# Kernel tuning notes

Measured on AMD Instinct MI355X. Metric: run time of the kernel, lower is better.

Reference implementation:

```python
import jax, jax.numpy as jnp
import numpy as np

N = 40000
E = 640000
D_IN = 128
HID = 128


def _sage_conv(x_src, x_dst, edge_index, W_l, b_l, W_r):
    """PyG SAGEConv with mean aggregation.
    out = lin_l(mean_{j in N(i)} x_src[j]) + lin_r(x_dst[i])
    (lin_l carries the bias; lin_r has bias=False in PyG.)
    """
    src, dst = edge_index[0], edge_index[1]
    n = x_dst.shape[0]
    # gather neighbor (source) features, scatter-sum to targets
    msg_sum = jax.ops.segment_sum(x_src[src], dst, num_segments=n)  # [N, d]
    deg = jax.ops.segment_sum(jnp.ones((src.shape[0],), x_src.dtype), dst,
                              num_segments=n)  # [N]
    agg = msg_sum / jnp.maximum(deg, 1.0)[:, None]  # mean over in-neighbors
    return agg @ W_l + b_l + x_dst @ W_r


def setup_inputs() -> dict:
    key = jax.random.key(0)
    ks = jax.random.split(key, 8)
    s_in = 1.0 / np.sqrt(D_IN)
    s_h = 1.0 / np.sqrt(HID)
    return {
        "x": jax.random.normal(ks[0], (N, D_IN), jnp.float32),
        "edge_index": jax.random.randint(ks[1], (2, E), 0, N, jnp.int64)
                      if jax.config.jax_enable_x64 else
                      jax.random.randint(ks[1], (2, E), 0, N, jnp.int32),
        "W1_l": jax.random.normal(ks[2], (D_IN, HID), jnp.float32) * s_in,
        "b1": jax.random.normal(ks[3], (HID,), jnp.float32) * s_in,
        "W1_r": jax.random.normal(ks[4], (D_IN, HID), jnp.float32) * s_in,
        "W2_l": jax.random.normal(ks[5], (HID, HID), jnp.float32) * s_h,
        "b2": jax.random.normal(ks[6], (HID,), jnp.float32) * s_h,
        "W2_r": jax.random.normal(ks[7], (HID, HID), jnp.float32) * s_h,
    }


def reference(x, edge_index, W1_l, b1, W1_r, W2_l, b2, W2_r):
    h = _sage_conv(x, x, edge_index, W1_l, b1, W1_r)
    h = jax.nn.relu(h)
    out = _sage_conv(h, h, edge_index, W2_l, b2, W2_r)
    return out
```

## Files before the change

### kernel.cpp

```cpp
#include <hip/hip_runtime.h>
#include <hip/hip_bf16.h>

#define NN 40000
#define NE 640000
#define DD 128
#define SLOT 128

typedef unsigned short u16;
typedef unsigned int u32;
typedef __attribute__((ext_vector_type(8))) short short8v;
typedef __attribute__((ext_vector_type(4))) float f32x4;

__device__ __forceinline__ u16 f2b(float f) {
  __hip_bfloat16 h = __float2bfloat16(f);
  return *reinterpret_cast<u16*>(&h);
}

#define TOB_N (NN * DD / 4)
#define WCVT_N 65536
__global__ void setup_kernel(const float* __restrict__ x,
                             const float* __restrict__ W1l, const float* __restrict__ W1r,
                             const float* __restrict__ W2l, const float* __restrict__ W2r,
                             u16* __restrict__ xb, u16* __restrict__ wt1,
                             u16* __restrict__ wt2, int* __restrict__ cnt) {
  int i = blockIdx.x * 256 + threadIdx.x;
  if (i < TOB_N) {
    float4 v = *(const float4*)(x + (size_t)i * 4);
    ushort4 o;
    o.x = f2b(v.x); o.y = f2b(v.y); o.z = f2b(v.z); o.w = f2b(v.w);
    *(ushort4*)(xb + (size_t)i * 4) = o;
  } else if (i < TOB_N + WCVT_N) {
    int j = i - TOB_N;
    int layer = j >> 15;
    int jj = j & 32767;
    int n = jj >> 8, k = jj & 255;
    const float* W = layer ? ((k < 128) ? W2l : W2r) : ((k < 128) ? W1l : W1r);
    u16* Wt = layer ? wt2 : wt1;
    Wt[jj] = f2b(W[(size_t)(k & 127) * 128 + n]);
  } else if (i < TOB_N + WCVT_N + NN) {
    cnt[i - TOB_N - WCVT_N] = 0;
  }
}

__global__ void fill2_kernel(const int* __restrict__ src, const int* __restrict__ dst,
                             int* __restrict__ cnt, int* __restrict__ csr) {
  int e = blockIdx.x * 256 + threadIdx.x;
  if (e < NE) {
    int d = dst[e];
    int p = atomicAdd(&cnt[d], 1);
    if (p < SLOT) csr[(size_t)d * SLOT + p] = src[e];
  }
}

template <int OUT_BF16, int RELU>
__global__ __launch_bounds__(1024) void fused_kernel(
    const u16* __restrict__ feat, const int* __restrict__ cnt,
    const int* __restrict__ csr, const u16* __restrict__ Wt,
    const float* __restrict__ bias, void* __restrict__ outp) {
  __shared__ u16 As[2][16][128];
  const int t = threadIdx.x;
  const int wv = t >> 6;
  const int lane = t & 63;
  const int li = lane & 15;
  const int eo = lane >> 4;
  const int node = blockIdx.x * 16 + wv;
  const int swz = (wv & 7) << 4;

  const int deg = cnt[node];
  const int n = (deg < SLOT) ? deg : SLOT;
  const float inv = 1.0f / (float)(deg > 1 ? deg : 1);

  if (eo == 1) {
    const uint4 s = *(const uint4*)(feat + (size_t)node * DD + li * 8);
    *(uint4*)((char*)&As[1][wv][0] + ((li * 16) ^ swz)) = s;
  }

  float acc[8] = {0.f, 0.f, 0.f, 0.f, 0.f, 0.f, 0.f, 0.f};
  const int* crow = csr + (size_t)node * SLOT;
  for (int e = eo; e < n; e += 4) {
    const int srcn = crow[e];
    const uint4 v = *(const uint4*)(feat + (size_t)srcn * DD + li * 8);
    acc[0] += __uint_as_float(v.x << 16);
    acc[1] += __uint_as_float(v.x & 0xffff0000u);
    acc[2] += __uint_as_float(v.y << 16);
    acc[3] += __uint_as_float(v.y & 0xffff0000u);
    acc[4] += __uint_as_float(v.z << 16);
    acc[5] += __uint_as_float(v.z & 0xffff0000u);
    acc[6] += __uint_as_float(v.w << 16);
    acc[7] += __uint_as_float(v.w & 0xffff0000u);
  }
#pragma unroll
  for (int j = 0; j < 8; ++j) acc[j] += __shfl_xor(acc[j], 16, 64);
#pragma unroll
  for (int j = 0; j < 8; ++j) acc[j] += __shfl_xor(acc[j], 32, 64);
  if (eo == 0) {
    u16 r8[8];
#pragma unroll
    for (int j = 0; j < 8; ++j) r8[j] = f2b(acc[j] * inv);
    uint4 o;
    o.x = (u32)r8[0] | ((u32)r8[1] << 16);
    o.y = (u32)r8[2] | ((u32)r8[3] << 16);
    o.z = (u32)r8[4] | ((u32)r8[5] << 16);
    o.w = (u32)r8[6] | ((u32)r8[7] << 16);
    *(uint4*)((char*)&As[0][wv][0] + ((li * 16) ^ swz)) = o;
  }
  __syncthreads();

  if (wv < 8) {
    const int r = li;
    const int g = eo;
    f32x4 acc2 = (f32x4){0.f, 0.f, 0.f, 0.f};
#pragma unroll
    for (int ks = 0; ks < 8; ++ks) {
      const int sel = ks >> 2;
      const int c0 = (ks & 3) * 32 + g * 8;
      const short8v afr =
          *(const short8v*)((const char*)&As[sel][r][0] + ((c0 * 2) ^ ((r & 7) << 4)));
      const short8v bfr =
          *(const short8v*)(Wt + (size_t)(wv * 16 + r) * 256 + ks * 32 + g * 8);
      acc2 = __builtin_amdgcn_mfma_f32_16x16x32_bf16(afr, bfr, acc2, 0, 0, 0);
    }
    const int col = wv * 16 + r;
    const float bv = bias[col];
#pragma unroll
    for (int reg = 0; reg < 4; ++reg) {
      const int row = blockIdx.x * 16 + g * 4 + reg;
      float o = acc2[reg] + bv;
      if (RELU) o = fmaxf(o, 0.f);
      if (OUT_BF16)
        ((u16*)outp)[(size_t)row * DD + col] = f2b(o);
      else
        ((float*)outp)[(size_t)row * DD + col] = o;
    }
  }
}

extern "C" void kernel_launch(void* const* d_in, const int* in_sizes, int n_in,
                              void* d_out, int out_size, void* d_ws, size_t ws_size,
                              hipStream_t stream) {
  const float* x = (const float*)d_in[0];
  const int* ei = (const int*)d_in[1];
  const int* srcv = ei;
  const int* dstv = ei + NE;
  const float* W1l = (const float*)d_in[2];
  const float* b1 = (const float*)d_in[3];
  const float* W1r = (const float*)d_in[4];
  const float* W2l = (const float*)d_in[5];
  const float* b2 = (const float*)d_in[6];
  const float* W2r = (const float*)d_in[7];
  float* out = (float*)d_out;

  char* ws = (char*)d_ws;
  int* cnt = (int*)(ws + 0);
  int* csr = (int*)(ws + 160256);
  u16* xb = (u16*)(ws + 20640256);
  u16* hb = (u16*)(ws + 30880256);
  u16* wt1 = (u16*)(ws + 41120256);
  u16* wt2 = (u16*)(ws + 41185792);

  const int nbS = (TOB_N + WCVT_N + NN + 255) / 256;
  const int nbE = NE / 256;

  setup_kernel<<<nbS, 256, 0, stream>>>(x, W1l, W1r, W2l, W2r, xb, wt1, wt2, cnt);
  fill2_kernel<<<nbE, 256, 0, stream>>>(srcv, dstv, cnt, csr);
  fused_kernel<1, 1><<<NN / 16, 1024, 0, stream>>>(xb, cnt, csr, wt1, b1, (void*)hb);
  fused_kernel<0, 0><<<NN / 16, 1024, 0, stream>>>(hb, cnt, csr, wt2, b2, (void*)out);
}
```

Measured before the change: 137.6 us.

## Process four nodes per wave in fused SAGE kernel with 256-thread blocks

Each wave now aggregates four destination nodes at once, keeping four sets of accumulators and issuing four independent gathers per iteration. Missing neighbours point at a zeroed padding row, which replaces per-edge branching. The block shrinks to 256 threads, and every wave now computes two MFMA column tiles instead of half the waves sitting idle. CSR writes become nontemporal stores. The intent is more memory-level parallelism and better MFMA utilisation, at the cost of higher register pressure and wasted loads when the four nodes have very different degrees.

```diff
diff --git a/kernel.cpp b/kernel.cpp
--- a/kernel.cpp
+++ b/kernel.cpp
@@ -22,7 +22,8 @@
                              const float* __restrict__ W1l, const float* __restrict__ W1r,
                              const float* __restrict__ W2l, const float* __restrict__ W2r,
                              u16* __restrict__ xb, u16* __restrict__ wt1,
-                             u16* __restrict__ wt2, int* __restrict__ cnt) {
+                             u16* __restrict__ wt2, int* __restrict__ cnt,
+                             u16* __restrict__ hb) {
   int i = blockIdx.x * 256 + threadIdx.x;
   if (i < TOB_N) {
     float4 v = *(const float4*)(x + (size_t)i * 4);
@@ -39,6 +40,11 @@
     Wt[jj] = f2b(W[(size_t)(k & 127) * 128 + n]);
   } else if (i < TOB_N + WCVT_N + NN) {
     cnt[i - TOB_N - WCVT_N] = 0;
+  } else if (i < TOB_N + WCVT_N + NN + 128) {
+    int j = i - TOB_N - WCVT_N - NN;
+    u32* p = (j < 64) ? ((u32*)(xb + (size_t)NN * DD) + j)
+                      : ((u32*)(hb + (size_t)NN * DD) + (j - 64));
+    *p = 0u;
   }
 }
 
@@ -48,84 +54,118 @@
   if (e < NE) {
     int d = dst[e];
     int p = atomicAdd(&cnt[d], 1);
-    if (p < SLOT) csr[(size_t)d * SLOT + p] = src[e];
+    if (p < SLOT) __builtin_nontemporal_store(src[e], &csr[(size_t)d * SLOT + p]);
   }
 }
 
 template <int OUT_BF16, int RELU>
-__global__ __launch_bounds__(1024) void fused_kernel(
+__global__ __launch_bounds__(256) void fused_kernel(
     const u16* __restrict__ feat, const int* __restrict__ cnt,
     const int* __restrict__ csr, const u16* __restrict__ Wt,
     const float* __restrict__ bias, void* __restrict__ outp) {
   __shared__ u16 As[2][16][128];
   const int t = threadIdx.x;
-  const int wv = t >> 6;
+  const int w = t >> 6;
   const int lane = t & 63;
   const int li = lane & 15;
   const int eo = lane >> 4;
-  const int node = blockIdx.x * 16 + wv;
-  const int swz = (wv & 7) << 4;
-
-  const int deg = cnt[node];
-  const int n = (deg < SLOT) ? deg : SLOT;
-  const float inv = 1.0f / (float)(deg > 1 ? deg : 1);
-
-  if (eo == 1) {
-    const uint4 s = *(const uint4*)(feat + (size_t)node * DD + li * 8);
-    *(uint4*)((char*)&As[1][wv][0] + ((li * 16) ^ swz)) = s;
-  }
-
-  float acc[8] = {0.f, 0.f, 0.f, 0.f, 0.f, 0.f, 0.f, 0.f};
-  const int* crow = csr + (size_t)node * SLOT;
-  for (int e = eo; e < n; e += 4) {
-    const int srcn = crow[e];
-    const uint4 v = *(const uint4*)(feat + (size_t)srcn * DD + li * 8);
-    acc[0] += __uint_as_float(v.x << 16);
-    acc[1] += __uint_as_float(v.x & 0xffff0000u);
-    acc[2] += __uint_as_float(v.y << 16);
-    acc[3] += __uint_as_float(v.y & 0xffff0000u);
-    acc[4] += __uint_as_float(v.z << 16);
-    acc[5] += __uint_as_float(v.z & 0xffff0000u);
-    acc[6] += __uint_as_float(v.w << 16);
-    acc[7] += __uint_as_float(v.w & 0xffff0000u);
-  }
-#pragma unroll
-  for (int j = 0; j < 8; ++j) acc[j] += __shfl_xor(acc[j], 16, 64);
-#pragma unroll
-  for (int j = 0; j < 8; ++j) acc[j] += __shfl_xor(acc[j], 32, 64);
+  const int tile = blockIdx.x * 16;
+  const int node0 = tile + w * 4;
+
+  {
+    const int j = w * 4 + eo;
+    const uint4 s = *(const uint4*)(feat + (size_t)(tile + j) * DD + li * 8);
+    *(uint4*)((char*)&As[1][j][0] + ((li * 16) ^ ((j & 7) << 4))) = s;
+  }
+
+  int n[4];
+  float inv[4];
+#pragma unroll
+  for (int s = 0; s < 4; ++s) {
+    const int d = cnt[node0 + s];
+    n[s] = (d < SLOT) ? d : SLOT;
+    inv[s] = 1.0f / (float)(d > 1 ? d : 1);
+  }
+  int nmax = max(max(n[0], n[1]), max(n[2], n[3]));
+
+  float acc[4][8];
+#pragma unroll
+  for (int s = 0; s < 4; ++s)
+#pragma unroll
+    for (int j = 0; j < 8; ++j) acc[s][j] = 0.f;
+
+  const int* crow0 = csr + (size_t)node0 * SLOT;
+  for (int it = eo; it < nmax; it += 4) {
+    int srcn[4];
+#pragma unroll
+    for (int s = 0; s < 4; ++s)
+      srcn[s] = (it < n[s]) ? crow0[s * SLOT + it] : NN;
+    uint4 v[4];
+#pragma unroll
+    for (int s = 0; s < 4; ++s)
+      v[s] = *(const uint4*)(feat + (size_t)srcn[s] * DD + li * 8);
+#pragma unroll
+    for (int s = 0; s < 4; ++s) {
+      acc[s][0] += __uint_as_float(v[s].x << 16);
+      acc[s][1] += __uint_as_float(v[s].x & 0xffff0000u);
+      acc[s][2] += __uint_as_float(v[s].y << 16);
+      acc[s][3] += __uint_as_float(v[s].y & 0xffff0000u);
+      acc[s][4] += __uint_as_float(v[s].z << 16);
+      acc[s][5] += __uint_as_float(v[s].z & 0xffff0000u);
+      acc[s][6] += __uint_as_float(v[s].w << 16);
+      acc[s][7] += __uint_as_float(v[s].w & 0xffff0000u);
+    }
+  }
+#pragma unroll
+  for (int s = 0; s < 4; ++s)
+#pragma unroll
+    for (int j = 0; j < 8; ++j) {
+      acc[s][j] += __shfl_xor(acc[s][j], 16, 64);
+      acc[s][j] += __shfl_xor(acc[s][j], 32, 64);
+    }
   if (eo == 0) {
-    u16 r8[8];
-#pragma unroll
-    for (int j = 0; j < 8; ++j) r8[j] = f2b(acc[j] * inv);
-    uint4 o;
-    o.x = (u32)r8[0] | ((u32)r8[1] << 16);
-    o.y = (u32)r8[2] | ((u32)r8[3] << 16);
-    o.z = (u32)r8[4] | ((u32)r8[5] << 16);
-    o.w = (u32)r8[6] | ((u32)r8[7] << 16);
-    *(uint4*)((char*)&As[0][wv][0] + ((li * 16) ^ swz)) = o;
+#pragma unroll
+    for (int s = 0; s < 4; ++s) {
+      u16 r8[8];
+#pragma unroll
+      for (int j = 0; j < 8; ++j) r8[j] = f2b(acc[s][j] * inv[s]);
+      uint4 o;
+      o.x = (u32)r8[0] | ((u32)r8[1] << 16);
+      o.y = (u32)r8[2] | ((u32)r8[3] << 16);
+      o.z = (u32)r8[4] | ((u32)r8[5] << 16);
+      o.w = (u32)r8[6] | ((u32)r8[7] << 16);
+      const int j = w * 4 + s;
+      *(uint4*)((char*)&As[0][j][0] + ((li * 16) ^ ((j & 7) << 4))) = o;
+    }
   }
   __syncthreads();
 
-  if (wv < 8) {
-    const int r = li;
-    const int g = eo;
-    f32x4 acc2 = (f32x4){0.f, 0.f, 0.f, 0.f};
-#pragma unroll
-    for (int ks = 0; ks < 8; ++ks) {
-      const int sel = ks >> 2;
-      const int c0 = (ks & 3) * 32 + g * 8;
-      const short8v afr =
-          *(const short8v*)((const char*)&As[sel][r][0] + ((c0 * 2) ^ ((r & 7) << 4)));
-      const short8v bfr =
-          *(const short8v*)(Wt + (size_t)(wv * 16 + r) * 256 + ks * 32 + g * 8);
-      acc2 = __builtin_amdgcn_mfma_f32_16x16x32_bf16(afr, bfr, acc2, 0, 0, 0);
-    }
-    const int col = wv * 16 + r;
+  const int r = li;
+  const int g = eo;
+  f32x4 acc2[2];
+  acc2[0] = (f32x4){0.f, 0.f, 0.f, 0.f};
+  acc2[1] = (f32x4){0.f, 0.f, 0.f, 0.f};
+#pragma unroll
+  for (int ks = 0; ks < 8; ++ks) {
+    const int sel = ks >> 2;
+    const int c0 = (ks & 3) * 32 + g * 8;
+    const short8v afr =
+        *(const short8v*)((const char*)&As[sel][r][0] + ((c0 * 2) ^ ((r & 7) << 4)));
+#pragma unroll
+    for (int ntl = 0; ntl < 2; ++ntl) {
+      const int col = (w * 2 + ntl) * 16 + r;
+      const short8v bfr = *(const short8v*)(Wt + (size_t)col * 256 + ks * 32 + g * 8);
+      acc2[ntl] = __builtin_amdgcn_mfma_f32_16x16x32_bf16(afr, bfr, acc2[ntl], 0, 0, 0);
+    }
+  }
+#pragma unroll
+  for (int ntl = 0; ntl < 2; ++ntl) {
+    const int col = (w * 2 + ntl) * 16 + r;
     const float bv = bias[col];
 #pragma unroll
     for (int reg = 0; reg < 4; ++reg) {
-      const int row = blockIdx.x * 16 + g * 4 + reg;
-      float o = acc2[reg] + bv;
+      const int row = tile + g * 4 + reg;
+      float o = acc2[ntl][reg] + bv;
       if (RELU) o = fmaxf(o, 0.f);
       if (OUT_BF16)
         ((u16*)outp)[(size_t)row * DD + col] = f2b(o);
@@ -154,15 +194,15 @@
   int* cnt = (int*)(ws + 0);
   int* csr = (int*)(ws + 160256);
   u16* xb = (u16*)(ws + 20640256);
-  u16* hb = (u16*)(ws + 30880256);
-  u16* wt1 = (u16*)(ws + 41120256);
-  u16* wt2 = (u16*)(ws + 41185792);
-
-  const int nbS = (TOB_N + WCVT_N + NN + 255) / 256;
+  u16* hb = (u16*)(ws + 30880512);
+  u16* wt1 = (u16*)(ws + 41120768);
+  u16* wt2 = (u16*)(ws + 41186304);
+
+  const int nbS = (TOB_N + WCVT_N + NN + 128 + 255) / 256;
   const int nbE = NE / 256;
 
-  setup_kernel<<<nbS, 256, 0, stream>>>(x, W1l, W1r, W2l, W2r, xb, wt1, wt2, cnt);
+  setup_kernel<<<nbS, 256, 0, stream>>>(x, W1l, W1r, W2l, W2r, xb, wt1, wt2, cnt, hb);
   fill2_kernel<<<nbE, 256, 0, stream>>>(srcv, dstv, cnt, csr);
-  fused_kernel<1, 1><<<NN / 16, 1024, 0, stream>>>(xb, cnt, csr, wt1, b1, (void*)hb);
-  fused_kernel<0, 0><<<NN / 16, 1024, 0, stream>>>(hb, cnt, csr, wt2, b2, (void*)out);
-}
+  fused_kernel<1, 1><<<NN / 16, 256, 0, stream>>>(xb, cnt, csr, wt1, b1, (void*)hb);
+  fused_kernel<0, 0><<<NN / 16, 256, 0, stream>>>(hb, cnt, csr, wt2, b2, (void*)out);
+}
```

Result: slower. 144.0 us (+4.6%).
